# Performance work log

Measured on AMD Instinct MI355X. Metric: run time of the kernel, lower is better.

Reference implementation:

```python
import jax, jax.numpy as jnp
import numpy as np

B, N, D, E = 8, 512, 64, 32

def setup_inputs() -> dict:
    key = jax.random.key(0)
    k1, k2, k3 = jax.random.split(key, 3)
    x = jax.random.normal(k1, (B, N, D), dtype=jnp.float32)
    We = jax.random.normal(k2, (2 * D, E), dtype=jnp.float32) * (1.0 / np.sqrt(2 * D))
    be = jnp.zeros((E,), dtype=jnp.float32)
    Wr = jax.random.normal(k3, (N * E, 1), dtype=jnp.float32) * (1.0 / np.sqrt(N * E))
    br = jnp.zeros((1,), dtype=jnp.float32)
    return {"x": x, "We": We, "be": be, "Wr": Wr, "br": br}

def reference(x, We, be, Wr, br):
    b, n, d = x.shape
    # cat([x_i, x_j]) @ We == x_i @ We[:d] + x_j @ We[d:]  (avoids materializing the concat)
    W_src, W_dst = We[:d], We[d:]
    src = jnp.einsum('bid,de->bie', x, W_src)   # [B,N,E] contribution of start node i
    dst = jnp.einsum('bjd,de->bje', x, W_dst)   # [B,N,E] contribution of terminal node j
    edges = jax.nn.relu(src[:, :, None, :] + dst[:, None, :, :] + be)  # [B,N,N,E] edge (i->j)
    incoming = jnp.swapaxes(edges, 1, 2)        # [B, N(dst), N(src), E] permute(0,2,1,3)
    agg = incoming.reshape(b, n, n * edges.shape[-1])  # [B,N,N*E]
    delta = agg @ Wr + br                       # [B,N,1]
    return delta
```

## Files before the change

kernel.cpp:

```cpp
#include <hip/hip_runtime.h>

#define BNE (4096 * 32)

__global__ __launch_bounds__(64) void proj_kernel(
    const float* __restrict__ x, const float* __restrict__ We,
    const float* __restrict__ be, const float* __restrict__ br,
    float* __restrict__ out, float* __restrict__ ws)
{
    const int lane = threadIdx.x;
    const int row  = blockIdx.x;
    const int proj = lane >> 5;
    const int e    = lane & 31;

    const float* __restrict__ xrow = x + (size_t)row * 64;
    const float* __restrict__ wcol = We + proj * (64 * 32) + e;

    float acc = 0.0f;
    #pragma unroll
    for (int d = 0; d < 64; ++d)
        acc = fmaf(xrow[d], wcol[d * 32], acc);

    if (proj == 0) acc += be[e];

    ws[(size_t)proj * BNE + (size_t)row * 32 + e] = acc;

    if (blockIdx.x < 64) out[blockIdx.x * 64 + lane] = br[0];
}

__global__ __launch_bounds__(256) void edge_kernel(
    const float* __restrict__ ws, const float* __restrict__ Wr,
    float* __restrict__ out)
{
    const float* __restrict__ src = ws;
    const float* __restrict__ dst = ws + BNE;

    const int b  = blockIdx.z;
    const int j0 = threadIdx.x;
    const int j1 = threadIdx.x + 256;
    const int i0 = blockIdx.x * 8;

    float d0[32], d1[32];
    const float4* __restrict__ dp0 = (const float4*)(dst + ((size_t)(b * 512 + j0)) * 32);
    const float4* __restrict__ dp1 = (const float4*)(dst + ((size_t)(b * 512 + j1)) * 32);
    #pragma unroll
    for (int k = 0; k < 8; ++k) {
        ((float4*)d0)[k] = dp0[k];
        ((float4*)d1)[k] = dp1[k];
    }

    float a00 = 0.f, a01 = 0.f, a10 = 0.f, a11 = 0.f;

    #pragma unroll 2
    for (int ii = 0; ii < 8; ++ii) {
        const int i = i0 + ii;
        const float* __restrict__ srow = src + ((size_t)(b * 512 + i)) * 32;
        const float* __restrict__ wrow = Wr + (size_t)i * 32;
        #pragma unroll
        for (int e = 0; e < 32; e += 2) {
            const float s0 = srow[e],  s1 = srow[e + 1];
            const float w0 = wrow[e],  w1 = wrow[e + 1];
            float t00 = fmaxf(s0 + d0[e],     0.f);
            float t01 = fmaxf(s1 + d0[e + 1], 0.f);
            float t10 = fmaxf(s0 + d1[e],     0.f);
            float t11 = fmaxf(s1 + d1[e + 1], 0.f);
            a00 = fmaf(t00, w0, a00);
            a01 = fmaf(t01, w1, a01);
            a10 = fmaf(t10, w0, a10);
            a11 = fmaf(t11, w1, a11);
        }
    }

    atomicAdd(&out[b * 512 + j0], a00 + a01);
    atomicAdd(&out[b * 512 + j1], a10 + a11);
}

extern "C" void kernel_launch(void* const* d_in, const int* in_sizes, int n_in,
                              void* d_out, int out_size, void* d_ws, size_t ws_size,
                              hipStream_t stream) {
    const float* x  = (const float*)d_in[0];
    const float* We = (const float*)d_in[1];
    const float* be = (const float*)d_in[2];
    const float* Wr = (const float*)d_in[3];
    const float* br = (const float*)d_in[4];
    float* out = (float*)d_out;
    float* ws  = (float*)d_ws;

    proj_kernel<<<4096, 64, 0, stream>>>(x, We, be, br, out, ws);
    edge_kernel<<<dim3(64, 1, 8), 256, 0, stream>>>(ws, Wr, out);
}
```

Measured before the change: 73.31 us.

## Retile edge kernel: 4 destination nodes per thread, 4 sources per block

The edge kernel now launches 1024 blocks of 128 threads instead of 512 blocks of 256. Each thread keeps four destination rows in registers instead of two, and each block handles four source nodes instead of eight. The source and Wr rows are read as float4, so each broadcast load feeds four accumulators. The aim is more parallelism across CUs and more reuse of each loaded value. The costs are about 128 registers per thread for the destination rows, twice as many atomics on the output, and a possible loss of occupancy.

Measured after the change: 79.59 us. 1.09x slower.

```diff
diff --git a/kernel.cpp b/kernel.cpp
--- a/kernel.cpp
+++ b/kernel.cpp
@@ -27,51 +27,60 @@
     if (blockIdx.x < 64) out[blockIdx.x * 64 + lane] = br[0];
 }
 
-__global__ __launch_bounds__(256) void edge_kernel(
+__global__ __launch_bounds__(128, 2) void edge_kernel(
     const float* __restrict__ ws, const float* __restrict__ Wr,
     float* __restrict__ out)
 {
     const float* __restrict__ src = ws;
     const float* __restrict__ dst = ws + BNE;
 
-    const int b  = blockIdx.z;
-    const int j0 = threadIdx.x;
-    const int j1 = threadIdx.x + 256;
-    const int i0 = blockIdx.x * 8;
+    const int t  = threadIdx.x;
+    const int b  = blockIdx.y;
+    const int i0 = blockIdx.x * 4;
 
-    float d0[32], d1[32];
-    const float4* __restrict__ dp0 = (const float4*)(dst + ((size_t)(b * 512 + j0)) * 32);
-    const float4* __restrict__ dp1 = (const float4*)(dst + ((size_t)(b * 512 + j1)) * 32);
+    float d[4][32];
     #pragma unroll
-    for (int k = 0; k < 8; ++k) {
-        ((float4*)d0)[k] = dp0[k];
-        ((float4*)d1)[k] = dp1[k];
-    }
-
-    float a00 = 0.f, a01 = 0.f, a10 = 0.f, a11 = 0.f;
-
-    #pragma unroll 2
-    for (int ii = 0; ii < 8; ++ii) {
-        const int i = i0 + ii;
-        const float* __restrict__ srow = src + ((size_t)(b * 512 + i)) * 32;
-        const float* __restrict__ wrow = Wr + (size_t)i * 32;
+    for (int jj = 0; jj < 4; ++jj) {
+        const int j = t + jj * 128;
+        const float4* __restrict__ dp =
+            (const float4*)(dst + ((size_t)(b * 512 + j)) * 32);
         #pragma unroll
-        for (int e = 0; e < 32; e += 2) {
-            const float s0 = srow[e],  s1 = srow[e + 1];
-            const float w0 = wrow[e],  w1 = wrow[e + 1];
-            float t00 = fmaxf(s0 + d0[e],     0.f);
-            float t01 = fmaxf(s1 + d0[e + 1], 0.f);
-            float t10 = fmaxf(s0 + d1[e],     0.f);
-            float t11 = fmaxf(s1 + d1[e + 1], 0.f);
-            a00 = fmaf(t00, w0, a00);
-            a01 = fmaf(t01, w1, a01);
-            a10 = fmaf(t10, w0, a10);
-            a11 = fmaf(t11, w1, a11);
+        for (int k = 0; k < 8; ++k) {
+            const float4 v = dp[k];
+            d[jj][k * 4 + 0] = v.x;
+            d[jj][k * 4 + 1] = v.y;
+            d[jj][k * 4 + 2] = v.z;
+            d[jj][k * 4 + 3] = v.w;
         }
     }
 
-    atomicAdd(&out[b * 512 + j0], a00 + a01);
-    atomicAdd(&out[b * 512 + j1], a10 + a11);
+    float acc[4] = {0.f, 0.f, 0.f, 0.f};
+
+    #pragma unroll
+    for (int ii = 0; ii < 4; ++ii) {
+        const int i = i0 + ii;
+        const float4* __restrict__ s4 =
+            (const float4*)(src + ((size_t)(b * 512 + i)) * 32);
+        const float4* __restrict__ w4 =
+            (const float4*)(Wr + (size_t)i * 32);
+        #pragma unroll
+        for (int q = 0; q < 8; ++q) {
+            const float4 s = s4[q];
+            const float4 w = w4[q];
+            const int e = q * 4;
+            #pragma unroll
+            for (int jj = 0; jj < 4; ++jj) {
+                acc[jj] = fmaf(fmaxf(s.x + d[jj][e + 0], 0.f), w.x, acc[jj]);
+                acc[jj] = fmaf(fmaxf(s.y + d[jj][e + 1], 0.f), w.y, acc[jj]);
+                acc[jj] = fmaf(fmaxf(s.z + d[jj][e + 2], 0.f), w.z, acc[jj]);
+                acc[jj] = fmaf(fmaxf(s.w + d[jj][e + 3], 0.f), w.w, acc[jj]);
+            }
+        }
+    }
+
+    #pragma unroll
+    for (int jj = 0; jj < 4; ++jj)
+        atomicAdd(&out[b * 512 + t + jj * 128], acc[jj]);
 }
 
 extern "C" void kernel_launch(void* const* d_in, const int* in_sizes, int n_in,
@@ -86,5 +95,5 @@
     float* ws  = (float*)d_ws;
 
     proj_kernel<<<4096, 64, 0, stream>>>(x, We, be, br, out, ws);
-    edge_kernel<<<dim3(64, 1, 8), 256, 0, stream>>>(ws, Wr, out);
+    edge_kernel<<<dim3(128, 8), 128, 0, stream>>>(ws, Wr, out);
 }
```
